# Optimization experiments

Measured on AMD Instinct MI355X. Metric: run time of the kernel, lower is better.

Reference implementation:

```python
import jax, jax.numpy as jnp
import numpy as np

D = 1024
H = 16
HD = D // H
B, K, S = 2, 1024, 4096
EPS = 1e-5


def _ln(x, w, b):
    mu = jnp.mean(x, axis=-1, keepdims=True)
    var = jnp.mean((x - mu) ** 2, axis=-1, keepdims=True)
    return (x - mu) * jax.lax.rsqrt(var + EPS) * w + b


def setup_inputs() -> dict:
    key = jax.random.key(0)
    ks = jax.random.split(key, 16)
    p = lambda k, shape: jax.random.normal(k, shape, dtype=jnp.float32) * 0.02
    return {
        "q": jax.random.normal(ks[0], (B, K, D), dtype=jnp.float32),
        "kv": jax.random.normal(ks[1], (B, S, D), dtype=jnp.float32),
        "attn_bias": jax.random.normal(ks[2], (B, K, S), dtype=jnp.float32),
        "obs_bias": jax.random.normal(ks[3], (B, K, S), dtype=jnp.float32),
        "density": jax.random.uniform(ks[4], (B, K), dtype=jnp.float32),
        "ln_q_w": jnp.ones((D,), jnp.float32), "ln_q_b": jnp.zeros((D,), jnp.float32),
        "ln_kv_w": jnp.ones((D,), jnp.float32), "ln_kv_b": jnp.zeros((D,), jnp.float32),
        "wq": p(ks[5], (D, D)), "bq": jnp.zeros((D,), jnp.float32),
        "wk": p(ks[6], (D, D)), "bk": jnp.zeros((D,), jnp.float32),
        "wv": p(ks[7], (D, D)), "bv": jnp.zeros((D,), jnp.float32),
        "wo": p(ks[8], (D, D)), "bo": jnp.zeros((D,), jnp.float32),
        "dist_raw": jnp.float32(0.0),
        "obs_raw": jnp.float32(0.0),
        "dens_raw": jnp.float32(0.0),
        "ln_f_w": jnp.ones((D,), jnp.float32), "ln_f_b": jnp.zeros((D,), jnp.float32),
        "w1": p(ks[9], (D, 2 * D)), "b1": jnp.zeros((2 * D,), jnp.float32),
        "w2": p(ks[10], (2 * D, D)), "b2": jnp.zeros((D,), jnp.float32),
    }


def reference(q, kv, attn_bias, obs_bias, density,
              ln_q_w, ln_q_b, ln_kv_w, ln_kv_b,
              wq, bq, wk, bk, wv, bv, wo, bo,
              dist_raw, obs_raw, dens_raw,
              ln_f_w, ln_f_b, w1, b1, w2, b2):
    b, k, _ = q.shape
    s = kv.shape[1]
    scale = HD ** (-0.5)

    q_in = _ln(q, ln_q_w, ln_q_b)
    kv_in = _ln(kv, ln_kv_w, ln_kv_b)

    # [B, H, K, HD] / [B, H, S, HD]
    qp = (q_in @ wq + bq).reshape(b, k, H, HD).transpose(0, 2, 1, 3)
    kp = (kv_in @ wk + bk).reshape(b, s, H, HD).transpose(0, 2, 1, 3)
    vp = (kv_in @ wv + bv).reshape(b, s, H, HD).transpose(0, 2, 1, 3)

    scores = jnp.einsum('bhkd,bhsd->bhks', qp, kp) * scale
    scores = scores + jax.nn.softplus(dist_raw) * attn_bias[:, None]
    scores = scores + jax.nn.softplus(obs_raw) * obs_bias[:, None]
    gate = 1.0 + jnp.tanh(dens_raw) * density[:, None, :, None]  # [B,1,K,1]
    scores = scores * gate

    attn = jax.nn.softmax(scores, axis=-1)  # dropout is identity at eval
    out = jnp.einsum('bhks,bhsd->bhkd', attn, vp)
    out = out.transpose(0, 2, 1, 3).reshape(b, k, D) @ wo + bo

    x = q + out
    h = jax.nn.gelu(_ln(x, ln_f_w, ln_f_b) @ w1 + b1, approximate=False)
    x = x + (h @ w2 + b2)
    return x
```

## Files before the change

kernel.cpp:

```cpp
#include <hip/hip_runtime.h>
#include <cstdint>

#define DEV __device__ __forceinline__

typedef __attribute__((ext_vector_type(8))) short bfx8;
typedef __attribute__((ext_vector_type(4))) short bfx4;
typedef __attribute__((ext_vector_type(4))) float fx4;
typedef unsigned short u16;

constexpr int DIM = 1024, NH = 16, HD = 64, BB = 2, KQ = 1024, SEQ = 4096;

DEV u16 f2bf(float f) {
    union { float f; unsigned u; } v{f};
    unsigned r = (v.u + 0x7fffu + ((v.u >> 16) & 1u)) >> 16;
    return (u16)r;
}
DEV float bf2f(u16 s) {
    union { unsigned u; float f; } v{(unsigned)s << 16};
    return v.f;
}
DEV float softplus_f(float x) { return x > 20.f ? x : log1pf(expf(x)); }

#define GLDS(gp, lp)                                                        \
    __builtin_amdgcn_global_load_lds(                                       \
        (const __attribute__((address_space(1))) void*)(gp),                \
        (__attribute__((address_space(3))) void*)(lp), 16, 0, 0)

__global__ __launch_bounds__(256) void wt_kernel(const float* __restrict__ W,
                                                 u16* __restrict__ Wt,
                                                 int Kd, int N) {
    __shared__ float tile[32][33];
    const int k0 = blockIdx.y * 32, n0 = blockIdx.x * 32;
    const int r = threadIdx.x >> 3, c4 = (threadIdx.x & 7) * 4;
    float4 v = *(const float4*)&W[(long)(k0 + r) * N + n0 + c4];
    tile[r][c4 + 0] = v.x; tile[r][c4 + 1] = v.y;
    tile[r][c4 + 2] = v.z; tile[r][c4 + 3] = v.w;
    __syncthreads();
    bfx4 o;
#pragma unroll
    for (int j = 0; j < 4; j++) o[j] = f2bf(tile[c4 + j][r]);
    *(bfx4*)&Wt[(long)(n0 + r) * Kd + k0 + c4] = o;
}

__global__ __launch_bounds__(256) void combine_bias(const float* __restrict__ ab,
                                                    const float* __restrict__ ob,
                                                    const float* __restrict__ dist_raw,
                                                    const float* __restrict__ obs_raw,
                                                    u16* __restrict__ cb) {
    const float c1 = softplus_f(dist_raw[0]), c2 = softplus_f(obs_raw[0]);
    long i = (long)blockIdx.x * 256 + threadIdx.x;
    float4 a = ((const float4*)ab)[i];
    float4 o = ((const float4*)ob)[i];
    bfx4 r;
    r[0] = f2bf(c1 * a.x + c2 * o.x);
    r[1] = f2bf(c1 * a.y + c2 * o.y);
    r[2] = f2bf(c1 * a.z + c2 * o.z);
    r[3] = f2bf(c1 * a.w + c2 * o.w);
    ((bfx4*)cb)[i] = r;
}

__global__ __launch_bounds__(256) void ln_kernel(const float* __restrict__ x,
                                                 const float* __restrict__ w,
                                                 const float* __restrict__ bsh,
                                                 u16* __restrict__ out) {
    const long row = blockIdx.x;
    const float4 v = ((const float4*)(x + row * DIM))[threadIdx.x];
    float s1 = v.x + v.y + v.z + v.w;
    float s2 = v.x * v.x + v.y * v.y + v.z * v.z + v.w * v.w;
#pragma unroll
    for (int off = 32; off > 0; off >>= 1) {
        s1 += __shfl_xor(s1, off, 64);
        s2 += __shfl_xor(s2, off, 64);
    }
    __shared__ float red[2][4];
    if ((threadIdx.x & 63) == 0) {
        red[0][threadIdx.x >> 6] = s1;
        red[1][threadIdx.x >> 6] = s2;
    }
    __syncthreads();
    s1 = red[0][0] + red[0][1] + red[0][2] + red[0][3];
    s2 = red[1][0] + red[1][1] + red[1][2] + red[1][3];
    float mu = s1 * (1.f / DIM);
    float var = s2 * (1.f / DIM) - mu * mu;
    float rs = rsqrtf(var + 1e-5f);
    int c = threadIdx.x * 4;
    float4 wv = ((const float4*)w)[threadIdx.x];
    float4 bv = ((const float4*)bsh)[threadIdx.x];
    bfx4 o;
    o[0] = f2bf((v.x - mu) * rs * wv.x + bv.x);
    o[1] = f2bf((v.y - mu) * rs * wv.y + bv.y);
    o[2] = f2bf((v.z - mu) * rs * wv.z + bv.z);
    o[3] = f2bf((v.w - mu) * rs * wv.w + bv.w);
    *(bfx4*)&out[row * DIM + c] = o;
}

template <int NT, class Epi>
__global__ __launch_bounds__(256) void gemm_bt(const u16* __restrict__ A,
                                               const u16* __restrict__ Bt,
                                               int Kd, Epi epi) {
    constexpr int NB = NT / 32;
    __shared__ u16 As[128 * 64];
    __shared__ u16 Bs[NT * 64];
    const int tid = threadIdx.x;
    const int lane = tid & 63, wave = tid >> 6;
    const int quad = lane >> 4, l16 = lane & 15;
    const int wm = (wave >> 1) * 64, wn = (wave & 1) * (NT / 2);
    const long row0 = (long)blockIdx.y * 128, col0 = (long)blockIdx.x * NT;
    const int lr = lane >> 3;
    const int lch = (lane & 7) ^ lr;
    const int sw = (l16 & 7);

    fx4 acc[4][NB] = {};
    for (int k0 = 0; k0 < Kd; k0 += 64) {
        __syncthreads();
#pragma unroll
        for (int p = 0; p < 4; p++) {
            int ch = wave * 4 + p;
            GLDS(&A[(row0 + ch * 8 + lr) * Kd + k0 + lch * 8], &As[ch * 512]);
        }
#pragma unroll
        for (int p = 0; p < NB; p++) {
            int ch = wave * NB + p;
            GLDS(&Bt[(col0 + ch * 8 + lr) * Kd + k0 + lch * 8], &Bs[ch * 512]);
        }
        __syncthreads();
        bfx8 af[2][4], bfv[2][NB];
#pragma unroll
        for (int kk = 0; kk < 2; kk++) {
#pragma unroll
            for (int m = 0; m < 4; m++)
                af[kk][m] = *(const bfx8*)&As[(wm + m * 16 + l16) * 64 +
                                              (((kk * 4 + quad) ^ sw) * 8)];
#pragma unroll
            for (int n = 0; n < NB; n++)
                bfv[kk][n] = *(const bfx8*)&Bs[(wn + n * 16 + l16) * 64 +
                                               (((kk * 4 + quad) ^ sw) * 8)];
        }
#pragma unroll
        for (int kk = 0; kk < 2; kk++)
#pragma unroll
            for (int m = 0; m < 4; m++)
#pragma unroll
                for (int n = 0; n < NB; n++)
                    acc[m][n] = __builtin_amdgcn_mfma_f32_16x16x32_bf16(
                        af[kk][m], bfv[kk][n], acc[m][n], 0, 0, 0);
    }
#pragma unroll
    for (int m = 0; m < 4; m++)
#pragma unroll
        for (int n = 0; n < NB; n++)
            epi((int)(row0 + wm + m * 16 + quad * 4),
                (int)(col0 + wn + n * 16 + l16), acc[m][n]);
}

struct EpiQp {
    const float* bias; u16* out;
    DEV void operator()(int r0, int c, fx4 v) const {
        float bv = bias[c];
#pragma unroll
        for (int r = 0; r < 4; r++)
            out[(long)(r0 + r) * DIM + c] = f2bf((v[r] + bv) * 0.125f);
    }
};
struct EpiBias16 {
    const float* bias; u16* out;
    DEV void operator()(int r0, int c, fx4 v) const {
        float bv = bias[c];
#pragma unroll
        for (int r = 0; r < 4; r++)
            out[(long)(r0 + r) * DIM + c] = f2bf(v[r] + bv);
    }
};
struct EpiVpT {
    const float* bias; u16* vpT;
    DEV void operator()(int r0, int c, fx4 v) const {
        float bv = bias[c];
        int b = r0 >> 12, s = r0 & (SEQ - 1);
        bfx4 o;
#pragma unroll
        for (int r = 0; r < 4; r++) o[r] = f2bf(v[r] + bv);
        *(bfx4*)&vpT[((long)(b * DIM + c)) * SEQ + s] = o;
    }
};
struct EpiWo {
    const float* bias; const float* qres; float* x;
    DEV void operator()(int r0, int c, fx4 v) const {
        float bv = bias[c];
#pragma unroll
        for (int r = 0; r < 4; r++) {
            long idx = (long)(r0 + r) * DIM + c;
            x[idx] = qres[idx] + v[r] + bv;
        }
    }
};
struct EpiW1 {
    const float* bias; u16* h;
    DEV void operator()(int r0, int c, fx4 v) const {
        float bv = bias[c];
#pragma unroll
        for (int r = 0; r < 4; r++) {
            float t = v[r] + bv;
            float g = 0.5f * t * (1.f + erff(t * 0.70710678118654752f));
            h[(long)(r0 + r) * (2 * DIM) + c] = f2bf(g);
        }
    }
};
struct EpiW2 {
    const float* bias; const float* x; float* out;
    DEV void operator()(int r0, int c, fx4 v) const {
        float bv = bias[c];
#pragma unroll
        for (int r = 0; r < 4; r++) {
            long idx = (long)(r0 + r) * DIM + c;
            out[idx] = x[idx] + v[r] + bv;
        }
    }
};

__global__ __launch_bounds__(256) void attn_kernel(
    const u16* __restrict__ qp, const u16* __restrict__ kp,
    const u16* __restrict__ vpT, const u16* __restrict__ cb,
    const float* __restrict__ density, const float* __restrict__ dens_raw,
    u16* __restrict__ attn_out) {
    const int b = blockIdx.z, h = blockIdx.y, q0 = blockIdx.x * 64;
    const int tid = threadIdx.x, wave = tid >> 6, lane = tid & 63;
    const int quad = lane >> 4, l16 = lane & 15;
    const int lr = lane >> 3, lch = (lane & 7) ^ lr, sw = l16 & 7;
    __shared__ u16 Qs[64 * 64], Ks[64 * 64], Vs[64 * 64];
    __shared__ u16 Ps[4][16][72];
    const float tgd = tanhf(dens_raw[0]);

#pragma unroll
    for (int p = 0; p < 2; p++) {
        int ch = wave * 2 + p;
        GLDS(&qp[((long)(b * KQ + q0 + ch * 8 + lr)) * DIM + h * HD + lch * 8],
             &Qs[ch * 512]);
    }
    const int qrow = q0 + wave * 16 + quad * 4;
    float gate[4];
#pragma unroll
    for (int r = 0; r < 4; r++)
        gate[r] = 1.f + tgd * density[b * KQ + qrow + r];
    __syncthreads();

    bfx8 aq[2];
#pragma unroll
    for (int kk = 0; kk < 2; kk++)
        aq[kk] = *(const bfx8*)&Qs[(wave * 16 + l16) * 64 +
                                   (((kk * 4 + quad) ^ sw) * 8)];

    float lsum[4] = {};
    fx4 O[4] = {};
    const u16* cbr[4];
#pragma unroll
    for (int r = 0; r < 4; r++)
        cbr[r] = cb + (long)(b * KQ) * SEQ + (long)(qrow + r) * SEQ + l16;

    for (int s0 = 0; s0 < SEQ; s0 += 64) {
        __syncthreads();
#pragma unroll
        for (int p = 0; p < 2; p++) {
            int ch = wave * 2 + p;
            GLDS(&kp[((long)(b * SEQ + s0 + ch * 8 + lr)) * DIM + h * HD + lch * 8],
                 &Ks[ch * 512]);
            GLDS(&vpT[((long)(b * DIM + h * HD + ch * 8 + lr)) * SEQ + s0 + lch * 8],
                 &Vs[ch * 512]);
        }
        u16 cbv[4][4];
#pragma unroll
        for (int sb = 0; sb < 4; sb++)
#pragma unroll
            for (int r = 0; r < 4; r++)
                cbv[sb][r] = cbr[r][s0 + sb * 16];
        __syncthreads();
        fx4 sc[4] = {};
#pragma unroll
        for (int sb = 0; sb < 4; sb++)
#pragma unroll
            for (int kk = 0; kk < 2; kk++) {
                bfx8 bk = *(const bfx8*)&Ks[(sb * 16 + l16) * 64 +
                                            (((kk * 4 + quad) ^ sw) * 8)];
                sc[sb] = __builtin_amdgcn_mfma_f32_16x16x32_bf16(aq[kk], bk, sc[sb], 0, 0, 0);
            }
#pragma unroll
        for (int sb = 0; sb < 4; sb++)
#pragma unroll
            for (int r = 0; r < 4; r++) {
                float e = __expf((sc[sb][r] + bf2f(cbv[sb][r])) * gate[r]);
                lsum[r] += e;
                Ps[wave][quad * 4 + r][sb * 16 + l16] = f2bf(e);
            }
#pragma unroll
        for (int kk = 0; kk < 2; kk++) {
            bfx8 ap = *(const bfx8*)&Ps[wave][l16][kk * 32 + quad * 8];
#pragma unroll
            for (int d = 0; d < 4; d++) {
                bfx8 bv = *(const bfx8*)&Vs[(d * 16 + l16) * 64 +
                                            (((kk * 4 + quad) ^ sw) * 8)];
                O[d] = __builtin_amdgcn_mfma_f32_16x16x32_bf16(ap, bv, O[d], 0, 0, 0);
            }
        }
    }
#pragma unroll
    for (int off = 1; off < 16; off <<= 1)
#pragma unroll
        for (int r = 0; r < 4; r++)
            lsum[r] += __shfl_xor(lsum[r], off, 16);
    float inv[4];
#pragma unroll
    for (int r = 0; r < 4; r++) inv[r] = 1.f / lsum[r];
#pragma unroll
    for (int d = 0; d < 4; d++)
#pragma unroll
        for (int r = 0; r < 4; r++)
            attn_out[((long)(b * KQ + qrow + r)) * DIM + h * HD + d * 16 + l16] =
                f2bf(O[d][r] * inv[r]);
}

extern "C" void kernel_launch(void* const* d_in, const int* in_sizes, int n_in,
                              void* d_out, int out_size, void* d_ws, size_t ws_size,
                              hipStream_t stream) {
    (void)in_sizes; (void)n_in; (void)out_size; (void)ws_size;
    const float* q        = (const float*)d_in[0];
    const float* kv       = (const float*)d_in[1];
    const float* ab       = (const float*)d_in[2];
    const float* ob       = (const float*)d_in[3];
    const float* dens     = (const float*)d_in[4];
    const float* lnqw     = (const float*)d_in[5];
    const float* lnqb     = (const float*)d_in[6];
    const float* lnkw     = (const float*)d_in[7];
    const float* lnkb     = (const float*)d_in[8];
    const float* wq       = (const float*)d_in[9];
    const float* bq       = (const float*)d_in[10];
    const float* wk       = (const float*)d_in[11];
    const float* bk       = (const float*)d_in[12];
    const float* wv       = (const float*)d_in[13];
    const float* bv       = (const float*)d_in[14];
    const float* wo       = (const float*)d_in[15];
    const float* bo       = (const float*)d_in[16];
    const float* dist_raw = (const float*)d_in[17];
    const float* obs_raw  = (const float*)d_in[18];
    const float* dens_raw = (const float*)d_in[19];
    const float* lnfw     = (const float*)d_in[20];
    const float* lnfb     = (const float*)d_in[21];
    const float* w1       = (const float*)d_in[22];
    const float* b1       = (const float*)d_in[23];
    const float* w2       = (const float*)d_in[24];
    const float* b2       = (const float*)d_in[25];
    float* out = (float*)d_out;

    char* ws = (char*)d_ws;
    const size_t MB = 1u << 20;
    u16* q_in  = (u16*)(ws + 0);
    u16* kv_in = (u16*)(ws + 4 * MB);
    u16* wq_t  = (u16*)(ws + 20 * MB);
    u16* wk_t  = (u16*)(ws + 22 * MB);
    u16* wv_t  = (u16*)(ws + 24 * MB);
    u16* wo_t  = (u16*)(ws + 26 * MB);
    u16* w1_t  = (u16*)(ws + 28 * MB);
    u16* w2_t  = (u16*)(ws + 32 * MB);
    u16* qp    = (u16*)(ws + 36 * MB);
    u16* kp    = (u16*)(ws + 40 * MB);
    u16* vpT   = (u16*)(ws + 56 * MB);
    u16* cbuf  = (u16*)(ws + 72 * MB);
    u16* aout  = (u16*)(ws + 88 * MB);
    float* xb  = (float*)(ws + 92 * MB);
    u16* xn    = (u16*)(ws + 100 * MB);
    u16* hbuf  = (u16*)(ws + 104 * MB);

    wt_kernel<<<dim3(DIM / 32, DIM / 32), 256, 0, stream>>>(wq, wq_t, DIM, DIM);
    wt_kernel<<<dim3(DIM / 32, DIM / 32), 256, 0, stream>>>(wk, wk_t, DIM, DIM);
    wt_kernel<<<dim3(DIM / 32, DIM / 32), 256, 0, stream>>>(wv, wv_t, DIM, DIM);
    wt_kernel<<<dim3(DIM / 32, DIM / 32), 256, 0, stream>>>(wo, wo_t, DIM, DIM);
    wt_kernel<<<dim3(2 * DIM / 32, DIM / 32), 256, 0, stream>>>(w1, w1_t, DIM, 2 * DIM);
    wt_kernel<<<dim3(DIM / 32, 2 * DIM / 32), 256, 0, stream>>>(w2, w2_t, 2 * DIM, DIM);
    combine_bias<<<(BB * KQ * (long)SEQ / 4) / 256, 256, 0, stream>>>(ab, ob, dist_raw, obs_raw, cbuf);
    ln_kernel<<<BB * KQ, 256, 0, stream>>>(q, lnqw, lnqb, q_in);
    ln_kernel<<<BB * SEQ, 256, 0, stream>>>(kv, lnkw, lnkb, kv_in);

    gemm_bt<64><<<dim3(DIM / 64, BB * KQ / 128), 256, 0, stream>>>(q_in, wq_t, DIM, EpiQp{bq, qp});
    gemm_bt<128><<<dim3(DIM / 128, BB * SEQ / 128), 256, 0, stream>>>(kv_in, wk_t, DIM, EpiBias16{bk, kp});
    gemm_bt<128><<<dim3(DIM / 128, BB * SEQ / 128), 256, 0, stream>>>(kv_in, wv_t, DIM, EpiVpT{bv, vpT});

    attn_kernel<<<dim3(KQ / 64, NH, BB), 256, 0, stream>>>(qp, kp, vpT, cbuf, dens, dens_raw, aout);

    gemm_bt<64><<<dim3(DIM / 64, BB * KQ / 128), 256, 0, stream>>>(aout, wo_t, DIM, EpiWo{bo, q, xb});
    ln_kernel<<<BB * KQ, 256, 0, stream>>>(xb, lnfw, lnfb, xn);
    gemm_bt<128><<<dim3(2 * DIM / 128, BB * KQ / 128), 256, 0, stream>>>(xn, w1_t, DIM, EpiW1{b1, hbuf});
    gemm_bt<64><<<dim3(DIM / 64, BB * KQ / 128), 256, 0, stream>>>(hbuf, w2_t, 2 * DIM, EpiW2{b2, xb, out});
}
```

Before: 485.6 us.

## Split attention over sequence halves, fuse KV GEMM, and keep P in registers

```diff
diff --git a/kernel.cpp b/kernel.cpp
--- a/kernel.cpp
+++ b/kernel.cpp
@@ -7,6 +7,7 @@
 typedef __attribute__((ext_vector_type(4))) short bfx4;
 typedef __attribute__((ext_vector_type(4))) float fx4;
 typedef unsigned short u16;
+typedef unsigned int u32;
 
 constexpr int DIM = 1024, NH = 16, HD = 64, BB = 2, KQ = 1024, SEQ = 4096;
 
@@ -46,16 +47,21 @@
                                                     const float* __restrict__ ob,
                                                     const float* __restrict__ dist_raw,
                                                     const float* __restrict__ obs_raw,
+                                                    const float* __restrict__ density,
+                                                    const float* __restrict__ dens_raw,
                                                     u16* __restrict__ cb) {
     const float c1 = softplus_f(dist_raw[0]), c2 = softplus_f(obs_raw[0]);
+    const float tgd = tanhf(dens_raw[0]);
     long i = (long)blockIdx.x * 256 + threadIdx.x;
+    int row = (int)(i >> 10);
+    float g = 1.f + tgd * density[row];
     float4 a = ((const float4*)ab)[i];
     float4 o = ((const float4*)ob)[i];
     bfx4 r;
-    r[0] = f2bf(c1 * a.x + c2 * o.x);
-    r[1] = f2bf(c1 * a.y + c2 * o.y);
-    r[2] = f2bf(c1 * a.z + c2 * o.z);
-    r[3] = f2bf(c1 * a.w + c2 * o.w);
+    r[0] = f2bf((c1 * a.x + c2 * o.x) * g);
+    r[1] = f2bf((c1 * a.y + c2 * o.y) * g);
+    r[2] = f2bf((c1 * a.z + c2 * o.z) * g);
+    r[3] = f2bf((c1 * a.w + c2 * o.w) * g);
     ((bfx4*)cb)[i] = r;
 }
 
@@ -94,61 +100,61 @@
     *(bfx4*)&out[row * DIM + c] = o;
 }
 
-template <int NT, class Epi>
+template <int MT, int NT, class Epi>
 __global__ __launch_bounds__(256) void gemm_bt(const u16* __restrict__ A,
                                                const u16* __restrict__ Bt,
                                                int Kd, Epi epi) {
-    constexpr int NB = NT / 32;
-    __shared__ u16 As[128 * 64];
+    constexpr int MF = MT / 32, NF = NT / 32;
+    __shared__ u16 As[MT * 64];
     __shared__ u16 Bs[NT * 64];
     const int tid = threadIdx.x;
     const int lane = tid & 63, wave = tid >> 6;
     const int quad = lane >> 4, l16 = lane & 15;
-    const int wm = (wave >> 1) * 64, wn = (wave & 1) * (NT / 2);
-    const long row0 = (long)blockIdx.y * 128, col0 = (long)blockIdx.x * NT;
+    const int wm = (wave >> 1) * (MT / 2), wn = (wave & 1) * (NT / 2);
+    const long row0 = (long)blockIdx.y * MT, col0 = (long)blockIdx.x * NT;
     const int lr = lane >> 3;
     const int lch = (lane & 7) ^ lr;
     const int sw = (l16 & 7);
 
-    fx4 acc[4][NB] = {};
+    fx4 acc[MF][NF] = {};
     for (int k0 = 0; k0 < Kd; k0 += 64) {
         __syncthreads();
 #pragma unroll
-        for (int p = 0; p < 4; p++) {
-            int ch = wave * 4 + p;
+        for (int p = 0; p < MF; p++) {
+            int ch = wave * MF + p;
             GLDS(&A[(row0 + ch * 8 + lr) * Kd + k0 + lch * 8], &As[ch * 512]);
         }
 #pragma unroll
-        for (int p = 0; p < NB; p++) {
-            int ch = wave * NB + p;
+        for (int p = 0; p < NF; p++) {
+            int ch = wave * NF + p;
             GLDS(&Bt[(col0 + ch * 8 + lr) * Kd + k0 + lch * 8], &Bs[ch * 512]);
         }
         __syncthreads();
-        bfx8 af[2][4], bfv[2][NB];
+        bfx8 af[2][MF], bfv[2][NF];
 #pragma unroll
         for (int kk = 0; kk < 2; kk++) {
 #pragma unroll
-            for (int m = 0; m < 4; m++)
+            for (int m = 0; m < MF; m++)
                 af[kk][m] = *(const bfx8*)&As[(wm + m * 16 + l16) * 64 +
                                               (((kk * 4 + quad) ^ sw) * 8)];
 #pragma unroll
-            for (int n = 0; n < NB; n++)
+            for (int n = 0; n < NF; n++)
                 bfv[kk][n] = *(const bfx8*)&Bs[(wn + n * 16 + l16) * 64 +
                                                (((kk * 4 + quad) ^ sw) * 8)];
         }
 #pragma unroll
         for (int kk = 0; kk < 2; kk++)
 #pragma unroll
-            for (int m = 0; m < 4; m++)
-#pragma unroll
-                for (int n = 0; n < NB; n++)
+            for (int m = 0; m < MF; m++)
+#pragma unroll
+                for (int n = 0; n < NF; n++)
                     acc[m][n] = __builtin_amdgcn_mfma_f32_16x16x32_bf16(
                         af[kk][m], bfv[kk][n], acc[m][n], 0, 0, 0);
     }
 #pragma unroll
-    for (int m = 0; m < 4; m++)
-#pragma unroll
-        for (int n = 0; n < NB; n++)
+    for (int m = 0; m < MF; m++)
+#pragma unroll
+        for (int n = 0; n < NF; n++)
             epi((int)(row0 + wm + m * 16 + quad * 4),
                 (int)(col0 + wn + n * 16 + l16), acc[m][n]);
 }
@@ -162,24 +168,23 @@
             out[(long)(r0 + r) * DIM + c] = f2bf((v[r] + bv) * 0.125f);
     }
 };
-struct EpiBias16 {
-    const float* bias; u16* out;
+struct EpiKV {
+    const float* bk; const float* bv; u16* kp; u16* vpT;
     DEV void operator()(int r0, int c, fx4 v) const {
-        float bv = bias[c];
-#pragma unroll
-        for (int r = 0; r < 4; r++)
-            out[(long)(r0 + r) * DIM + c] = f2bf(v[r] + bv);
-    }
-};
-struct EpiVpT {
-    const float* bias; u16* vpT;
-    DEV void operator()(int r0, int c, fx4 v) const {
-        float bv = bias[c];
-        int b = r0 >> 12, s = r0 & (SEQ - 1);
-        bfx4 o;
-#pragma unroll
-        for (int r = 0; r < 4; r++) o[r] = f2bf(v[r] + bv);
-        *(bfx4*)&vpT[((long)(b * DIM + c)) * SEQ + s] = o;
+        if (c < DIM) {
+            float b = bk[c];
+#pragma unroll
+            for (int r = 0; r < 4; r++)
+                kp[(long)(r0 + r) * DIM + c] = f2bf(v[r] + b);
+        } else {
+            int d = c - DIM;
+            float b = bv[d];
+            int bi = r0 >> 12, s = r0 & (SEQ - 1);
+            bfx4 o;
+#pragma unroll
+            for (int r = 0; r < 4; r++) o[r] = f2bf(v[r] + b);
+            *(bfx4*)&vpT[((long)(bi * DIM + d)) * SEQ + s] = o;
+        }
     }
 };
 struct EpiWo {
@@ -217,46 +222,42 @@
     }
 };
 
-__global__ __launch_bounds__(256) void attn_kernel(
+__global__ __launch_bounds__(256, 4) void attn_kernel(
     const u16* __restrict__ qp, const u16* __restrict__ kp,
     const u16* __restrict__ vpT, const u16* __restrict__ cb,
     const float* __restrict__ density, const float* __restrict__ dens_raw,
-    u16* __restrict__ attn_out) {
-    const int b = blockIdx.z, h = blockIdx.y, q0 = blockIdx.x * 64;
+    float* __restrict__ Opart, float* __restrict__ Lpart) {
+    const int b = blockIdx.z, h = blockIdx.y;
+    const int q0 = (blockIdx.x >> 1) * 64, sh = blockIdx.x & 1;
+    const int sbase = sh * (SEQ / 2);
     const int tid = threadIdx.x, wave = tid >> 6, lane = tid & 63;
     const int quad = lane >> 4, l16 = lane & 15;
     const int lr = lane >> 3, lch = (lane & 7) ^ lr, sw = l16 & 7;
-    __shared__ u16 Qs[64 * 64], Ks[64 * 64], Vs[64 * 64];
-    __shared__ u16 Ps[4][16][72];
+    __shared__ u16 QCb[64 * 64];
+    __shared__ u16 Ks[64 * 64], Vs[64 * 64];
     const float tgd = tanhf(dens_raw[0]);
 
 #pragma unroll
     for (int p = 0; p < 2; p++) {
         int ch = wave * 2 + p;
         GLDS(&qp[((long)(b * KQ + q0 + ch * 8 + lr)) * DIM + h * HD + lch * 8],
-             &Qs[ch * 512]);
-    }
-    const int qrow = q0 + wave * 16 + quad * 4;
-    float gate[4];
-#pragma unroll
-    for (int r = 0; r < 4; r++)
-        gate[r] = 1.f + tgd * density[b * KQ + qrow + r];
+             &QCb[ch * 512]);
+    }
+    const float gate = 1.f + tgd * density[b * KQ + q0 + wave * 16 + l16];
     __syncthreads();
-
-    bfx8 aq[2];
+    bfx8 bq[2];
 #pragma unroll
     for (int kk = 0; kk < 2; kk++)
-        aq[kk] = *(const bfx8*)&Qs[(wave * 16 + l16) * 64 +
-                                   (((kk * 4 + quad) ^ sw) * 8)];
-
-    float lsum[4] = {};
+        bq[kk] = *(const bfx8*)&QCb[(wave * 16 + l16) * 64 +
+                                    (((kk * 4 + quad) ^ sw) * 8)];
+
+    const int src0 = l16 + ((quad & 1) << 5);
+    const int src1 = src0 + 16;
+
+    float lsum = 0.f;
     fx4 O[4] = {};
-    const u16* cbr[4];
-#pragma unroll
-    for (int r = 0; r < 4; r++)
-        cbr[r] = cb + (long)(b * KQ) * SEQ + (long)(qrow + r) * SEQ + l16;
-
-    for (int s0 = 0; s0 < SEQ; s0 += 64) {
+
+    for (int s0 = sbase; s0 < sbase + SEQ / 2; s0 += 64) {
         __syncthreads();
 #pragma unroll
         for (int p = 0; p < 2; p++) {
@@ -265,56 +266,85 @@
                  &Ks[ch * 512]);
             GLDS(&vpT[((long)(b * DIM + h * HD + ch * 8 + lr)) * SEQ + s0 + lch * 8],
                  &Vs[ch * 512]);
-        }
-        u16 cbv[4][4];
-#pragma unroll
-        for (int sb = 0; sb < 4; sb++)
-#pragma unroll
-            for (int r = 0; r < 4; r++)
-                cbv[sb][r] = cbr[r][s0 + sb * 16];
+            GLDS(&cb[((long)(b * KQ + q0 + ch * 8 + lr)) * SEQ + s0 + lch * 8],
+                 &QCb[ch * 512]);
+        }
         __syncthreads();
         fx4 sc[4] = {};
 #pragma unroll
         for (int sb = 0; sb < 4; sb++)
 #pragma unroll
             for (int kk = 0; kk < 2; kk++) {
-                bfx8 bk = *(const bfx8*)&Ks[(sb * 16 + l16) * 64 +
+                bfx8 ak = *(const bfx8*)&Ks[(sb * 16 + l16) * 64 +
                                             (((kk * 4 + quad) ^ sw) * 8)];
-                sc[sb] = __builtin_amdgcn_mfma_f32_16x16x32_bf16(aq[kk], bk, sc[sb], 0, 0, 0);
+                sc[sb] = __builtin_amdgcn_mfma_f32_16x16x32_bf16(ak, bq[kk], sc[sb], 0, 0, 0);
             }
-#pragma unroll
-        for (int sb = 0; sb < 4; sb++)
+        u32 pr[4][2];
+#pragma unroll
+        for (int sb = 0; sb < 4; sb++) {
+            int cch = (sb * 2 + (quad >> 1)) ^ sw;
+            bfx4 cbv = *(const bfx4*)&QCb[(wave * 16 + l16) * 64 + cch * 8 + (quad & 1) * 4];
+            float e[4];
 #pragma unroll
             for (int r = 0; r < 4; r++) {
-                float e = __expf((sc[sb][r] + bf2f(cbv[sb][r])) * gate[r]);
-                lsum[r] += e;
-                Ps[wave][quad * 4 + r][sb * 16 + l16] = f2bf(e);
+                e[r] = __expf(fmaf(sc[sb][r], gate, bf2f(cbv[r])));
+                lsum += e[r];
             }
+            pr[sb][0] = __builtin_amdgcn_perm(
+                __builtin_bit_cast(u32, e[1]), __builtin_bit_cast(u32, e[0]), 0x07060302u);
+            pr[sb][1] = __builtin_amdgcn_perm(
+                __builtin_bit_cast(u32, e[3]), __builtin_bit_cast(u32, e[2]), 0x07060302u);
+        }
 #pragma unroll
         for (int kk = 0; kk < 2; kk++) {
-            bfx8 ap = *(const bfx8*)&Ps[wave][l16][kk * 32 + quad * 8];
+            u32 ap32[4];
+#pragma unroll
+            for (int rp = 0; rp < 2; rp++) {
+                u32 tmp = (quad & 2) ? pr[2 * kk + 1][rp] : pr[2 * kk][rp];
+                ap32[rp]     = (u32)__shfl((int)tmp, src0, 64);
+                ap32[2 + rp] = (u32)__shfl((int)tmp, src1, 64);
+            }
+            bfx8 ap = __builtin_bit_cast(bfx8, *(const __attribute__((ext_vector_type(4))) u32*)ap32);
 #pragma unroll
             for (int d = 0; d < 4; d++) {
-                bfx8 bv = *(const bfx8*)&Vs[(d * 16 + l16) * 64 +
-                                            (((kk * 4 + quad) ^ sw) * 8)];
-                O[d] = __builtin_amdgcn_mfma_f32_16x16x32_bf16(ap, bv, O[d], 0, 0, 0);
+                bfx8 bvv = *(const bfx8*)&Vs[(d * 16 + l16) * 64 +
+                                             (((kk * 4 + quad) ^ sw) * 8)];
+                O[d] = __builtin_amdgcn_mfma_f32_16x16x32_bf16(ap, bvv, O[d], 0, 0, 0);
             }
         }
     }
-#pragma unroll
-    for (int off = 1; off < 16; off <<= 1)
+    lsum += __shfl_xor(lsum, 16, 64);
+    lsum += __shfl_xor(lsum, 32, 64);
+    if (lane < 16)
+        Lpart[((long)sh * BB * NH + b * NH + h) * KQ + q0 + wave * 16 + lane] = lsum;
+    float* Op = Opart + (long)sh * BB * KQ * DIM;
+#pragma unroll
+    for (int d = 0; d < 4; d++)
 #pragma unroll
         for (int r = 0; r < 4; r++)
-            lsum[r] += __shfl_xor(lsum[r], off, 16);
-    float inv[4];
-#pragma unroll
-    for (int r = 0; r < 4; r++) inv[r] = 1.f / lsum[r];
-#pragma unroll
-    for (int d = 0; d < 4; d++)
-#pragma unroll
-        for (int r = 0; r < 4; r++)
-            attn_out[((long)(b * KQ + qrow + r)) * DIM + h * HD + d * 16 + l16] =
-                f2bf(O[d][r] * inv[r]);
+            Op[((long)(b * KQ + q0 + wave * 16 + quad * 4 + r)) * DIM +
+               h * HD + d * 16 + l16] = O[d][r];
+}
+
+__global__ __launch_bounds__(256) void attn_combine(
+    const float* __restrict__ Opart, const float* __restrict__ Lpart,
+    u16* __restrict__ aout) {
+    long i = (long)blockIdx.x * 256 + threadIdx.x;
+    long e = i * 4;
+    int row = (int)(e >> 10);
+    int h = ((int)e & 1023) >> 6;
+    int b = row >> 10, qq = row & 1023;
+    long li = ((long)(b * NH + h) << 10) + qq;
+    const long half = (long)BB * KQ * DIM;
+    float inv = 1.f / (Lpart[li] + Lpart[(long)BB * NH * KQ + li]);
+    float4 a = ((const float4*)Opart)[i];
+    float4 c = ((const float4*)(Opart + half))[i];
+    bfx4 o;
+    o[0] = f2bf((a.x + c.x) * inv);
+    o[1] = f2bf((a.y + c.y) * inv);
+    o[2] = f2bf((a.z + c.z) * inv);
+    o[3] = f2bf((a.w + c.w) * inv);
+    ((bfx4*)aout)[i] = o;
 }
 
 extern "C" void kernel_launch(void* const* d_in, const int* in_sizes, int n_in,
@@ -351,41 +381,49 @@
 
     char* ws = (char*)d_ws;
     const size_t MB = 1u << 20;
-    u16* q_in  = (u16*)(ws + 0);
-    u16* kv_in = (u16*)(ws + 4 * MB);
-    u16* wq_t  = (u16*)(ws + 20 * MB);
-    u16* wk_t  = (u16*)(ws + 22 * MB);
-    u16* wv_t  = (u16*)(ws + 24 * MB);
-    u16* wo_t  = (u16*)(ws + 26 * MB);
-    u16* w1_t  = (u16*)(ws + 28 * MB);
-    u16* w2_t  = (u16*)(ws + 32 * MB);
-    u16* qp    = (u16*)(ws + 36 * MB);
-    u16* kp    = (u16*)(ws + 40 * MB);
-    u16* vpT   = (u16*)(ws + 56 * MB);
-    u16* cbuf  = (u16*)(ws + 72 * MB);
-    u16* aout  = (u16*)(ws + 88 * MB);
-    float* xb  = (float*)(ws + 92 * MB);
-    u16* xn    = (u16*)(ws + 100 * MB);
-    u16* hbuf  = (u16*)(ws + 104 * MB);
+    u16* q_in   = (u16*)(ws + 0);
+    u16* kv_in  = (u16*)(ws + 4 * MB);
+    float* Opart = (float*)(ws + 0);
+    float* Lpart = (float*)(ws + 16 * MB);
+    u16* wq_t   = (u16*)(ws + 20 * MB);
+    u16* wkv_t  = (u16*)(ws + 22 * MB);
+    u16* wo_t   = (u16*)(ws + 26 * MB);
+    u16* w1_t   = (u16*)(ws + 28 * MB);
+    u16* w2_t   = (u16*)(ws + 32 * MB);
+    u16* qp     = (u16*)(ws + 36 * MB);
+    u16* kp     = (u16*)(ws + 40 * MB);
+    u16* vpT    = (u16*)(ws + 56 * MB);
+    u16* cbuf   = (u16*)(ws + 72 * MB);
+    u16* aout   = (u16*)(ws + 88 * MB);
+    float* xb   = (float*)(ws + 92 * MB);
+    u16* xn     = (u16*)(ws + 100 * MB);
+    u16* hbuf   = (u16*)(ws + 104 * MB);
 
     wt_kernel<<<dim3(DIM / 32, DIM / 32), 256, 0, stream>>>(wq, wq_t, DIM, DIM);
-    wt_kernel<<<dim3(DIM / 32, DIM / 32), 256, 0, stream>>>(wk, wk_t, DIM, DIM);
-    wt_kernel<<<dim3(DIM / 32, DIM / 32), 256, 0, stream>>>(wv, wv_t, DIM, DIM);
+    wt_kernel<<<dim3(DIM / 32, DIM / 32), 256, 0, stream>>>(wk, wkv_t, DIM, DIM);
+    wt_kernel<<<dim3(DIM / 32, DIM / 32), 256, 0, stream>>>(wv, wkv_t + (long)DIM * DIM, DIM, DIM);
     wt_kernel<<<dim3(DIM / 32, DIM / 32), 256, 0, stream>>>(wo, wo_t, DIM, DIM);
     wt_kernel<<<dim3(2 * DIM / 32, DIM / 32), 256, 0, stream>>>(w1, w1_t, DIM, 2 * DIM);
     wt_kernel<<<dim3(DIM / 32, 2 * DIM / 32), 256, 0, stream>>>(w2, w2_t, 2 * DIM, DIM);
-    combine_bias<<<(BB * KQ * (long)SEQ / 4) / 256, 256, 0, stream>>>(ab, ob, dist_raw, obs_raw, cbuf);
+    combine_bias<<<(BB * KQ * (long)SEQ / 4) / 256, 256, 0, stream>>>(
+        ab, ob, dist_raw, obs_raw, dens, dens_raw, cbuf);
     ln_kernel<<<BB * KQ, 256, 0, stream>>>(q, lnqw, lnqb, q_in);
     ln_kernel<<<BB * SEQ, 256, 0, stream>>>(kv, lnkw, lnkb, kv_in);
 
-    gemm_bt<64><<<dim3(DIM / 64, BB * KQ / 128), 256, 0, stream>>>(q_in, wq_t, DIM, EpiQp{bq, qp});
-    gemm_bt<128><<<dim3(DIM / 128, BB * SEQ / 128), 256, 0, stream>>>(kv_in, wk_t, DIM, EpiBias16{bk, kp});
-    gemm_bt<128><<<dim3(DIM / 128, BB * SEQ / 128), 256, 0, stream>>>(kv_in, wv_t, DIM, EpiVpT{bv, vpT});
-
-    attn_kernel<<<dim3(KQ / 64, NH, BB), 256, 0, stream>>>(qp, kp, vpT, cbuf, dens, dens_raw, aout);
-
-    gemm_bt<64><<<dim3(DIM / 64, BB * KQ / 128), 256, 0, stream>>>(aout, wo_t, DIM, EpiWo{bo, q, xb});
+    gemm_bt<64, 64><<<dim3(DIM / 64, BB * KQ / 64), 256, 0, stream>>>(
+        q_in, wq_t, DIM, EpiQp{bq, qp});
+    gemm_bt<128, 128><<<dim3(2 * DIM / 128, BB * SEQ / 128), 256, 0, stream>>>(
+        kv_in, wkv_t, DIM, EpiKV{bk, bv, kp, vpT});
+
+    attn_kernel<<<dim3(KQ / 64 * 2, NH, BB), 256, 0, stream>>>(
+        qp, kp, vpT, cbuf, dens, dens_raw, Opart, Lpart);
+    attn_combine<<<(BB * KQ * DIM / 4) / 256, 256, 0, stream>>>(Opart, Lpart, aout);
+
+    gemm_bt<64, 64><<<dim3(DIM / 64, BB * KQ / 64), 256, 0, stream>>>(
+        aout, wo_t, DIM, EpiWo{bo, q, xb});
     ln_kernel<<<BB * KQ, 256, 0, stream>>>(xb, lnfw, lnfb, xn);
-    gemm_bt<128><<<dim3(2 * DIM / 128, BB * KQ / 128), 256, 0, stream>>>(xn, w1_t, DIM, EpiW1{b1, hbuf});
-    gemm_bt<64><<<dim3(DIM / 64, BB * KQ / 128), 256, 0, stream>>>(hbuf, w2_t, 2 * DIM, EpiW2{b2, xb, out});
-}
+    gemm_bt<64, 128><<<dim3(2 * DIM / 128, BB * KQ / 64), 256, 0, stream>>>(
+        xn, w1_t, DIM, EpiW1{b1, hbuf});
+    gemm_bt<64, 64><<<dim3(DIM / 64, BB * KQ / 64), 256, 0, stream>>>(
+        hbuf, w2_t, 2 * DIM, EpiW2{b2, xb, out});
+}
```

Result: faster. 435.0 us (-10.4%).
